# Kernel tuning notes

Hardware: AMD Instinct MI355X
Metric: run time of the kernel (lower is better)

Reference implementation:

```python
import jax, jax.numpy as jnp
import numpy as np

T, DM = 2048, 2048
H, KV, D = 16, 2, 128
E, I_MOE, I_SH = 16, 768, 768
TOP_K, N_GROUP, TOPK_GROUP = 4, 4, 2
ROPE_THETA = 1e6
EPS = 1e-5
ROUTED_SCALE = 1.0


def rmsnorm(x, w):
    v = jnp.mean(x * x, axis=-1, keepdims=True)
    return x * jax.lax.rsqrt(v + EPS) * w


def apply_rope(x, pos):
    # partial rotary: first D//2 dims rotated (neox style), rest passthrough
    rd = D // 2
    half = rd // 2
    inv = 1.0 / (ROPE_THETA ** (jnp.arange(0, rd, 2, dtype=jnp.float32) / rd))
    freqs = pos.astype(jnp.float32)[:, None] * inv  # [T, half]
    cos = jnp.cos(freqs)[:, None, :]
    sin = jnp.sin(freqs)[:, None, :]
    x1, x2 = x[..., :half], x[..., half:rd]
    rot = jnp.concatenate([x1 * cos - x2 * sin, x2 * cos + x1 * sin], axis=-1)
    return jnp.concatenate([rot, x[..., rd:]], axis=-1)


def mlp(x, wgu, wd):
    g, u = jnp.split(x @ wgu, 2, axis=-1)
    return (jax.nn.silu(g) * u) @ wd


def attention(x, pos, w_qkv, b_qkv, w_o, q_norm_w, k_norm_w):
    qkv = x @ w_qkv + b_qkv
    q, k, v = jnp.split(qkv, [H * D, H * D + KV * D], axis=-1)
    q = rmsnorm(q.reshape(T, H, D), q_norm_w)
    k = rmsnorm(k.reshape(T, KV, D), k_norm_w)
    v = v.reshape(T, KV, D)
    q = apply_rope(q, pos)
    k = apply_rope(k, pos)
    rep = H // KV
    k = jnp.repeat(k, rep, axis=1)
    v = jnp.repeat(v, rep, axis=1)
    scores = jnp.einsum('thd,shd->hts', q, k) * (D ** -0.5)
    causal = pos[:, None] >= pos[None, :]
    scores = jnp.where(causal[None], scores, jnp.finfo(scores.dtype).min)
    p = jax.nn.softmax(scores, axis=-1)
    o = jnp.einsum('hts,shd->thd', p, v).reshape(T, H * D)
    return o @ w_o


def moe(x, gate_w, gate_bias, shared_wgu, shared_wd, expert_wgu, expert_wd):
    # sigmoid grouped top-k routing with e_score_correction_bias (DeepSeek/GLM style)
    logits = x.astype(jnp.float32) @ gate_w
    scores = jax.nn.sigmoid(logits)
    sb = scores + gate_bias
    g = sb.reshape(T, N_GROUP, E // N_GROUP)
    group_scores = jnp.sum(jax.lax.top_k(g, 2)[0], axis=-1)  # [T, n_group]
    _, gi = jax.lax.top_k(group_scores, TOPK_GROUP)
    gmask = jnp.zeros((T, N_GROUP)).at[jnp.arange(T)[:, None], gi].set(1.0)
    emask = jnp.repeat(gmask, E // N_GROUP, axis=1)
    masked = jnp.where(emask > 0, sb, -jnp.inf)
    _, idx = jax.lax.top_k(masked, TOP_K)  # [T, top_k]
    w = jnp.take_along_axis(scores, idx, axis=1)
    w = w / jnp.sum(w, axis=1, keepdims=True)  # renormalize (norm_topk_prob)
    cw = jnp.zeros((T, E)).at[jnp.arange(T)[:, None], idx].add(w)  # dense combine weights
    gu = jnp.einsum('td,edi->tei', x, expert_wgu)  # [T, E, 2I]
    gt, ut = jnp.split(gu, 2, axis=-1)
    act = jax.nn.silu(gt) * ut * cw[:, :, None]
    routed = jnp.einsum('tei,eid->td', act, expert_wd)
    shared = mlp(x, shared_wgu, shared_wd)
    return routed * ROUTED_SCALE + shared


def setup_inputs() -> dict:
    key = jax.random.key(0)
    ks = jax.random.split(key, 12)
    s = 0.02
    return {
        'positions': jnp.arange(T, dtype=jnp.int32),
        'hidden_states': jax.random.normal(ks[0], (T, DM), jnp.float32),
        'residual': jax.random.normal(ks[1], (T, DM), jnp.float32),
        'ln1_w': jnp.ones((DM,), jnp.float32),
        'ln2_w': jnp.ones((DM,), jnp.float32),
        'w_qkv': jax.random.normal(ks[2], (DM, (H + 2 * KV) * D), jnp.float32) * s,
        'b_qkv': jnp.zeros(((H + 2 * KV) * D,), jnp.float32),
        'w_o': jax.random.normal(ks[3], (H * D, DM), jnp.float32) * s,
        'q_norm_w': jnp.ones((D,), jnp.float32),
        'k_norm_w': jnp.ones((D,), jnp.float32),
        'gate_w': jax.random.normal(ks[4], (DM, E), jnp.float32) * s,
        'gate_bias': jax.random.normal(ks[5], (E,), jnp.float32) * 0.1,
        'shared_wgu': jax.random.normal(ks[6], (DM, 2 * I_SH), jnp.float32) * s,
        'shared_wd': jax.random.normal(ks[7], (I_SH, DM), jnp.float32) * s,
        'expert_wgu': jax.random.normal(ks[8], (E, DM, 2 * I_MOE), jnp.float32) * s,
        'expert_wd': jax.random.normal(ks[9], (E, I_MOE, DM), jnp.float32) * s,
    }


def reference(positions, hidden_states, residual, ln1_w, ln2_w, w_qkv, b_qkv, w_o,
              q_norm_w, k_norm_w, gate_w, gate_bias, shared_wgu, shared_wd,
              expert_wgu, expert_wd):
    # fused add + RMSNorm (residual is not None path)
    residual = hidden_states + residual
    h = rmsnorm(residual, ln1_w)
    h = attention(h, positions, w_qkv, b_qkv, w_o, q_norm_w, k_norm_w)
    residual = h + residual
    h = rmsnorm(residual, ln2_w)
    h = moe(h, gate_w, gate_bias, shared_wgu, shared_wd, expert_wgu, expert_wd)
    return h, residual
```

## Files before the change

### kernel.cpp

```cpp
#include <hip/hip_runtime.h>
#include <stdint.h>
#include <math.h>

#define T_ 2048
#define DM 2048
#define NH 16
#define NKV 2
#define HD 128
#define QKVN 2560
#define NE 16
#define IM 768
#define ISH 768
#define MAXROWS 10240
#define ROWS_ALL 12288
#define NBLK 136
#define SM_SCALE 0.08838834764831845f

typedef __attribute__((ext_vector_type(8))) short short8;
typedef __attribute__((ext_vector_type(4))) float f32x4;

__device__ __forceinline__ float bf2f(unsigned short u){ return __uint_as_float(((unsigned int)u)<<16); }
__device__ __forceinline__ unsigned short f2bf(float f){
  unsigned int u = __float_as_uint(f);
  return (unsigned short)((u + 0x7FFFu + ((u>>16)&1u)) >> 16);
}
__device__ __forceinline__ void split2(float x, unsigned short& hi, unsigned short& lo){
  hi = f2bf(x);
  lo = f2bf(x - bf2f(hi));
}

__device__ __forceinline__ void gload16(const void* g, void* l){
  __builtin_amdgcn_global_load_lds((const __attribute__((address_space(1))) unsigned int*)g,
                                   (__attribute__((address_space(3))) unsigned int*)l, 16, 0, 0);
}

__device__ __forceinline__ int xcd_swz(int bid, int nwg){
  int q = nwg >> 3, r = nwg & 7, x = bid & 7, p = bid >> 3;
  return (x < r ? x*(q+1) : r*(q+1) + (x-r)*q) + p;
}

#define BAR()    asm volatile("s_barrier" ::: "memory")
#define VW(N)    asm volatile("s_waitcnt vmcnt(" #N ")" ::: "memory")
#define LW0()    do{ asm volatile("s_waitcnt lgkmcnt(0)" ::: "memory"); __builtin_amdgcn_sched_barrier(0); }while(0)

template<bool ILV>
__global__ void k_tconv(const float* __restrict__ src, unsigned short* __restrict__ dst,
                        const float* __restrict__ srcS, unsigned short* __restrict__ dstS,
                        int R, int C, size_t sS, size_t sD){
  int z = blockIdx.z;
  if (srcS && z == gridDim.z-1){ src = srcS; dst = dstS; }
  else { src += (size_t)z * sS; dst += (size_t)z * sD; }
  __shared__ float tile[64*65];
  int tid = threadIdx.x;
  int r0 = blockIdx.y*64, c0 = blockIdx.x*64;
  int lr = tid>>4, lc = (tid&15)*4;
  #pragma unroll
  for (int j=0;j<4;j++){
    int row = j*16 + lr;
    float4 v = *(const float4*)&src[(size_t)(r0+row)*C + c0 + lc];
    float* t = &tile[row*65 + lc];
    t[0]=v.x; t[1]=v.y; t[2]=v.z; t[3]=v.w;
  }
  __syncthreads();
  #pragma unroll
  for (int jj=0;jj<2;jj++){
    int slot = jj*256 + tid;
    int c = slot>>3, ro = (slot&7)*8;
    int cg = c0 + c;
    int cd = cg;
    if (ILV){ int b = cg>>3, inner = cg&7; cd = (b<96 ? b*16 : (b-96)*16+8) + inner; }
    short8 o;
    #pragma unroll
    for (int k=0;k<8;k++) o[k] = (short)f2bf(tile[(ro+k)*65 + c]);
    *(short8*)&dst[(size_t)cd*R + r0 + ro] = o;
  }
}

__global__ void k_tconv2(const float* __restrict__ src, unsigned short* __restrict__ dhi,
                         unsigned short* __restrict__ dlo, int R, int C){
  __shared__ float tile[64*65];
  int tid = threadIdx.x;
  int r0 = blockIdx.y*64, c0 = blockIdx.x*64;
  int lr = tid>>4, lc = (tid&15)*4;
  #pragma unroll
  for (int j=0;j<4;j++){
    int row = j*16 + lr;
    float4 v = *(const float4*)&src[(size_t)(r0+row)*C + c0 + lc];
    float* t = &tile[row*65 + lc];
    t[0]=v.x; t[1]=v.y; t[2]=v.z; t[3]=v.w;
  }
  __syncthreads();
  #pragma unroll
  for (int jj=0;jj<2;jj++){
    int slot = jj*256 + tid;
    int c = slot>>3, ro = (slot&7)*8;
    short8 oh, ol;
    #pragma unroll
    for (int k=0;k<8;k++){
      unsigned short h_, l_;
      split2(tile[(ro+k)*65 + c], h_, l_);
      oh[k] = (short)h_; ol[k] = (short)l_;
    }
    size_t o = (size_t)(c0+c)*R + r0 + ro;
    *(short8*)&dhi[o] = oh;
    *(short8*)&dlo[o] = ol;
  }
}

template<bool ROUTE>
__global__ void k_add_rmsnorm(const float* __restrict__ a, const float* __restrict__ b,
                              const float* __restrict__ w, float* __restrict__ resout,
                              unsigned short* __restrict__ ohi, unsigned short* __restrict__ olo,
                              unsigned short* __restrict__ obf,
                              const float* __restrict__ gw, const float* __restrict__ gbias,
                              int* __restrict__ idx4, float* __restrict__ w4){
  int t = blockIdx.x, tid = threadIdx.x;
  const float4* a4 = (const float4*)(a + (size_t)t*DM);
  const float4* b4 = (const float4*)(b + (size_t)t*DM);
  float4 va = a4[tid], vb = b4[tid];
  float4 wa = a4[tid+256], wb = b4[tid+256];
  float4 v0, v1;
  v0.x=va.x+vb.x; v0.y=va.y+vb.y; v0.z=va.z+vb.z; v0.w=va.w+vb.w;
  v1.x=wa.x+wb.x; v1.y=wa.y+wb.y; v1.z=wa.z+wb.z; v1.w=wa.w+wb.w;
  float s = v0.x*v0.x+v0.y*v0.y+v0.z*v0.z+v0.w*v0.w
          + v1.x*v1.x+v1.y*v1.y+v1.z*v1.z+v1.w*v1.w;
  #pragma unroll
  for (int o=32;o;o>>=1) s += __shfl_xor(s,o);
  __shared__ float sm[4];
  if ((tid&63)==0) sm[tid>>6]=s;
  __syncthreads();
  s = sm[0]+sm[1]+sm[2]+sm[3];
  float rs = rsqrtf(s*(1.f/(float)DM) + 1e-5f);
  ((float4*)(resout + (size_t)t*DM))[tid] = v0;
  ((float4*)(resout + (size_t)t*DM))[tid+256] = v1;
  const float4* w4p_ = (const float4*)w;
  float4 w0 = w4p_[tid], w1 = w4p_[tid+256];
  float n[8] = { v0.x*rs*w0.x, v0.y*rs*w0.y, v0.z*rs*w0.z, v0.w*rs*w0.w,
                 v1.x*rs*w1.x, v1.y*rs*w1.y, v1.z*rs*w1.z, v1.w*rs*w1.w };
  if (ohi){
    ushort4 h0,h1,l0,l1;
    split2(n[0],h0.x,l0.x); split2(n[1],h0.y,l0.y); split2(n[2],h0.z,l0.z); split2(n[3],h0.w,l0.w);
    split2(n[4],h1.x,l1.x); split2(n[5],h1.y,l1.y); split2(n[6],h1.z,l1.z); split2(n[7],h1.w,l1.w);
    ((ushort4*)(ohi + (size_t)t*DM))[tid] = h0;
    ((ushort4*)(ohi + (size_t)t*DM))[tid+256] = h1;
    ((ushort4*)(olo + (size_t)t*DM))[tid] = l0;
    ((ushort4*)(olo + (size_t)t*DM))[tid+256] = l1;
  }
  if (obf){
    ushort4 o0 = make_ushort4(f2bf(n[0]),f2bf(n[1]),f2bf(n[2]),f2bf(n[3]));
    ushort4 o1 = make_ushort4(f2bf(n[4]),f2bf(n[5]),f2bf(n[6]),f2bf(n[7]));
    ((ushort4*)(obf + (size_t)t*DM))[tid] = o0;
    ((ushort4*)(obf + (size_t)t*DM))[tid+256] = o1;
  }
  if constexpr (ROUTE){
    __shared__ float xrow[DM];
    __shared__ float red[16][17];
    #pragma unroll
    for (int jj=0;jj<4;jj++) xrow[4*tid+jj] = n[jj];
    #pragma unroll
    for (int jj=0;jj<4;jj++) xrow[1024+4*tid+jj] = n[4+jj];
    __syncthreads();
    int e = tid & 15, grp = tid >> 4;
    float part = 0.f;
    #pragma unroll 8
    for (int c = grp; c < DM; c += 16)
      part += xrow[c] * gw[(size_t)c*16 + e];
    red[grp][e] = part;
    __syncthreads();
    if (tid==0){
      float sc[16], sb[16];
      for (int ee=0;ee<16;ee++){
        float lg = 0.f;
        for (int g2=0;g2<16;g2++) lg += red[g2][ee];
        sc[ee] = 1.f/(1.f+expf(-lg));
        sb[ee] = sc[ee] + gbias[ee];
      }
      float gs[4];
      for (int g=0;g<4;g++){
        float m1=-3.4e38f, m2=-3.4e38f;
        for (int j=0;j<4;j++){
          float v = sb[g*4+j];
          if (v>m1){ m2=m1; m1=v; } else if (v>m2) m2=v;
        }
        gs[g]=m1+m2;
      }
      int g1=0; for (int g=1;g<4;g++) if (gs[g]>gs[g1]) g1=g;
      int g2=-1; for (int g=0;g<4;g++){ if (g==g1) continue; if (g2<0 || gs[g]>gs[g2]) g2=g; }
      float msk[16];
      for (int ee=0;ee<16;ee++){ int g=ee>>2; msk[ee] = (g==g1||g==g2)? sb[ee] : -3.4e38f; }
      int id[4]; float wv[4]; float wsum=0.f;
      for (int s2=0;s2<4;s2++){
        int bb=0; float bv=-3.5e38f;
        for (int ee=0;ee<16;ee++) if (msk[ee]>bv){ bv=msk[ee]; bb=ee; }
        id[s2]=bb; wv[s2]=sc[bb]; wsum+=sc[bb]; msk[bb]=-3.5e38f;
      }
      float invs = 1.f/wsum;
      for (int s2=0;s2<4;s2++){
        idx4[t*4+s2]=id[s2];
        w4[t*4+s2]=wv[s2]*invs;
      }
    }
  }
}

template<bool GATHER, bool ACT>
__global__ __launch_bounds__(256) void k_gemm2(
    const unsigned short* __restrict__ A, const unsigned short* __restrict__ Be,
    const unsigned short* __restrict__ Bsh, unsigned short* __restrict__ C,
    int K, int lda, int ldb, int ldc,
    const int* __restrict__ offs, size_t sBe, const int* __restrict__ tok){
  int nx = gridDim.x;
  int nwg = nx * gridDim.y;
  int wid_ = xcd_swz(blockIdx.x + nx*blockIdx.y, nwg);
  int tN = wid_ % nx, tM = wid_ / nx;
  int rb = tM*128;
  if (rb >= offs[17]) return;
  const unsigned short* B;
  if (rb >= offs[16]) B = Bsh;
  else {
    int e=0;
    for (; e<15; ++e) if (offs[e+1] > rb) break;
    B = Be + (size_t)e*sBe;
  }
  __shared__ __align__(16) unsigned short As[2][4096];
  __shared__ __align__(16) unsigned short Bs[2][4096];
  int tid = threadIdx.x, lane = tid & 63, wwid = tid >> 6;
  int wr = wwid >> 1, wc = wwid & 1;
  const unsigned short* Bb = B + (size_t)tN*128*ldb;

  const unsigned short* Asrc0;
  const unsigned short* Asrc1;
  int r0s = tid>>2, r1s = r0s + 64;
  {
    if (GATHER){
      Asrc0 = A + (size_t)tok[rb + r0s]*lda;
      Asrc1 = A + (size_t)tok[rb + r1s]*lda;
    } else {
      Asrc0 = A + (size_t)(rb + r0s)*lda;
      Asrc1 = A + (size_t)(rb + r1s)*lda;
    }
  }
  int kc = tid&3;
  int sw = (r0s>>1)&3;
  int kcS = (kc ^ sw)*8;

  f32x4 acc[4][4];
  #pragma unroll
  for (int m=0;m<4;m++)
    #pragma unroll
    for (int n=0;n<4;n++) acc[m][n] = (f32x4){0.f,0.f,0.f,0.f};

  auto STAGE = [&](int b, int k0){
    gload16(Asrc0 + k0 + kcS, As[b] + (size_t)tid*8);
    gload16(Asrc1 + k0 + kcS, As[b] + (size_t)(256+tid)*8);
    gload16(Bb + (size_t)r0s*ldb + k0 + kcS, Bs[b] + (size_t)tid*8);
    gload16(Bb + (size_t)r1s*ldb + k0 + kcS, Bs[b] + (size_t)(256+tid)*8);
  };

  int nt = K >> 5, L = nt - 1;
  STAGE(0, 0);
  if (L >= 1) STAGE(1, 32);
  int i15 = lane & 15, g = lane >> 4;
  for (int i=0; i<nt; ++i){
    int cur = i & 1;
    if (i < L) { VW(4); } else { VW(0); }
    BAR();
    short8 af[4], bfr[4];
    #pragma unroll
    for (int m=0;m<4;m++){
      int row = wr*64 + m*16 + i15;
      int geff = g ^ ((row>>1)&3);
      af[m] = *(const short8*)(As[cur] + row*32 + geff*8);
    }
    #pragma unroll
    for (int n=0;n<4;n++){
      int row = wc*64 + n*16 + i15;
      int geff = g ^ ((row>>1)&3);
      bfr[n] = *(const short8*)(Bs[cur] + row*32 + geff*8);
    }
    LW0();
    BAR();
    if (i + 2 <= L) STAGE(cur, (i+2)*32);
    __builtin_amdgcn_s_setprio(1);
    #pragma unroll
    for (int m=0;m<4;m++)
      #pragma unroll
      for (int n=0;n<4;n++)
        acc[m][n] = __builtin_amdgcn_mfma_f32_16x16x32_bf16(af[m], bfr[n], acc[m][n], 0,0,0);
    __builtin_amdgcn_s_setprio(0);
  }

  if (ACT){
    int rbase = rb + wr*64, cb = tN*128 + wc*64;
    #pragma unroll
    for (int m=0;m<4;m++){
      int r0 = rbase + m*16 + ((lane>>4)<<2);
      #pragma unroll
      for (int n=0;n<4;n++){
        int f = ((cb + n*16)>>1) + (lane&7);
        #pragma unroll
        for (int r=0;r<4;r++){
          float v = acc[m][n][r];
          float vp = __shfl_xor(v, 8);
          if (!(lane&8)){
            float gg = v;
            float a = gg/(1.f+__expf(-gg))*vp;
            C[(size_t)(r0+r)*ldc + f] = f2bf(a);
          }
        }
      }
    }
  } else {
    int rbase = rb + wr*64, cb = tN*128 + wc*64;
    #pragma unroll
    for (int m=0;m<4;m++){
      int r0 = rbase + m*16 + ((lane>>4)<<2);
      #pragma unroll
      for (int n=0;n<4;n++){
        int c = cb + n*16 + (lane&15);
        #pragma unroll
        for (int r=0;r<4;r++) C[(size_t)(r0+r)*ldc + c] = f2bf(acc[m][n][r]);
      }
    }
  }
}

__global__ __launch_bounds__(256) void k_gemm_hp(
    const unsigned short* __restrict__ Ah, const unsigned short* __restrict__ Al,
    const unsigned short* __restrict__ Bh, const unsigned short* __restrict__ Bl,
    float* __restrict__ Cf,
    int K, int lda, int ldb, int ldc){
  int nx = gridDim.x, nwg = nx*gridDim.y;
  int w = xcd_swz(blockIdx.x + nx*blockIdx.y, nwg);
  int tN = w % nx, tM = w / nx;

  __shared__ __align__(16) unsigned short AsH[2][4096], AsL[2][4096];
  __shared__ __align__(16) unsigned short BsH[2][4096], BsL[2][4096];
  int tid = threadIdx.x, lane = tid & 63, wid = tid >> 6;
  int wr = wid >> 1, wc = wid & 1;
  const unsigned short* Abh = Ah + (size_t)tM*128*lda;
  const unsigned short* Abl = Al + (size_t)tM*128*lda;
  const unsigned short* Bbh = Bh + (size_t)tN*128*ldb;
  const unsigned short* Bbl = Bl + (size_t)tN*128*ldb;

  f32x4 acc[4][4];
  #pragma unroll
  for (int m=0;m<4;m++)
    #pragma unroll
    for (int n=0;n<4;n++) acc[m][n] = (f32x4){0.f,0.f,0.f,0.f};

  auto STAGE = [&](int b, int k0){
    #pragma unroll
    for (int j=0;j<2;j++){
      int cb = j*256 + tid;
      int row = cb>>2, kc = cb&3;
      int kcS = (kc ^ ((row>>1)&3))*8;
      size_t go = (size_t)row*lda + k0 + kcS;
      gload16(Abh + go, AsH[b] + (size_t)cb*8);
      gload16(Abl + go, AsL[b] + (size_t)cb*8);
      size_t bo = (size_t)row*ldb + k0 + kcS;
      gload16(Bbh + bo, BsH[b] + (size_t)cb*8);
      gload16(Bbl + bo, BsL[b] + (size_t)cb*8);
    }
  };

  int nt = K >> 5, L = nt - 1;
  STAGE(0, 0);
  if (L >= 1) STAGE(1, 32);
  int i15 = lane & 15, g = lane >> 4;
  for (int i=0; i<nt; ++i){
    int cur = i & 1;
    if (i < L) { VW(8); } else { VW(0); }
    BAR();
    short8 afh[4], afl[4], bfh[4], bfl[4];
    #pragma unroll
    for (int m=0;m<4;m++){
      int row = wr*64 + m*16 + i15;
      int ro = row*32 + (g ^ ((row>>1)&3))*8;
      afh[m] = *(const short8*)(AsH[cur] + ro);
      afl[m] = *(const short8*)(AsL[cur] + ro);
    }
    #pragma unroll
    for (int n=0;n<4;n++){
      int row = wc*64 + n*16 + i15;
      int ro = row*32 + (g ^ ((row>>1)&3))*8;
      bfh[n] = *(const short8*)(BsH[cur] + ro);
      bfl[n] = *(const short8*)(BsL[cur] + ro);
    }
    LW0();
    BAR();
    if (i + 2 <= L) STAGE(cur, (i+2)*32);
    __builtin_amdgcn_s_setprio(1);
    #pragma unroll
    for (int m=0;m<4;m++)
      #pragma unroll
      for (int n=0;n<4;n++){
        acc[m][n] = __builtin_amdgcn_mfma_f32_16x16x32_bf16(afh[m], bfh[n], acc[m][n], 0,0,0);
        acc[m][n] = __builtin_amdgcn_mfma_f32_16x16x32_bf16(afh[m], bfl[n], acc[m][n], 0,0,0);
        acc[m][n] = __builtin_amdgcn_mfma_f32_16x16x32_bf16(afl[m], bfh[n], acc[m][n], 0,0,0);
      }
    __builtin_amdgcn_s_setprio(0);
  }

  int rb = tM*128 + wr*64, cb = tN*128 + wc*64;
  #pragma unroll
  for (int m=0;m<4;m++){
    int r0 = rb + m*16 + ((lane>>4)<<2);
    #pragma unroll
    for (int n=0;n<4;n++){
      int c = cb + n*16 + (lane&15);
      #pragma unroll
      for (int r=0;r<4;r++) Cf[(size_t)(r0+r)*ldc + c] = acc[m][n][r];
    }
  }
}

__global__ __launch_bounds__(256) void k_qk_pers(
    const unsigned short* __restrict__ Qh, const unsigned short* __restrict__ Ql,
    const unsigned short* __restrict__ Kh, const unsigned short* __restrict__ Kl,
    float* __restrict__ Sp){
  int tM = blockIdx.x, z = blockIdx.y;
  int kvh = z >> 3;
  size_t tri = (size_t)tM*(tM+1)/2;
  const int ldq = NH*HD, ldk = NKV*HD;
  const unsigned short* Qbh = Qh + (size_t)(tM*128)*ldq + (size_t)z*HD;
  const unsigned short* Qbl = Ql + (size_t)(tM*128)*ldq + (size_t)z*HD;
  const unsigned short* Kbh = Kh + (size_t)kvh*HD;
  const unsigned short* Kbl = Kl + (size_t)kvh*HD;

  __shared__ __align__(16) unsigned short QsH[16384], QsL[16384];
  __shared__ __align__(16) unsigned short BsH[2][4096], BsL[2][4096];

  int tid = threadIdx.x, lane = tid & 63, wid = tid >> 6;
  int wr = wid >> 1, wc = wid & 1;
  int i15 = lane & 15, g = lane >> 4;

  #pragma unroll
  for (int j=0;j<8;j++){
    int gi = j*256 + tid;
    int chunk = gi >> 9;
    int row = (gi >> 2) & 127;
    int gg = gi & 3;
    int col = chunk*32 + (gg ^ ((row>>1)&3))*8;
    gload16(Qbh + (size_t)row*ldq + col, QsH + (size_t)gi*8);
    gload16(Qbl + (size_t)row*ldq + col, QsL + (size_t)gi*8);
  }

  auto BSTAGE = [&](int b, int ci){
    int tn = ci >> 2, c = ci & 3;
    const unsigned short* sh = Kbh + (size_t)(tn*128)*ldk;
    const unsigned short* sl = Kbl + (size_t)(tn*128)*ldk;
    #pragma unroll
    for (int j=0;j<2;j++){
      int gi = j*256 + tid;
      int row = gi >> 2, gg = gi & 3;
      int col = c*32 + (gg ^ ((row>>1)&3))*8;
      gload16(sh + (size_t)row*ldk + col, BsH[b] + (size_t)gi*8);
      gload16(sl + (size_t)row*ldk + col, BsL[b] + (size_t)gi*8);
    }
  };

  f32x4 acc[4][4];
  #pragma unroll
  for (int m=0;m<4;m++)
    #pragma unroll
    for (int n=0;n<4;n++) acc[m][n] = (f32x4){0.f,0.f,0.f,0.f};

  int NC = (tM+1)*4;
  BSTAGE(0, 0);
  BSTAGE(1, 1);
  for (int ci=0; ci<NC; ++ci){
    int cur = ci & 1, c = ci & 3, tn = ci >> 2;
    if (ci < NC-1) { VW(4); } else { VW(0); }
    BAR();
    short8 afh[4], afl[4], bfh[4], bfl[4];
    #pragma unroll
    for (int m=0;m<4;m++){
      int row = wr*64 + m*16 + i15;
      int ro = c*4096 + row*32 + (g ^ ((row>>1)&3))*8;
      afh[m] = *(const short8*)(QsH + ro);
      afl[m] = *(const short8*)(QsL + ro);
    }
    #pragma unroll
    for (int n=0;n<4;n++){
      int row = wc*64 + n*16 + i15;
      int ro = row*32 + (g ^ ((row>>1)&3))*8;
      bfh[n] = *(const short8*)(BsH[cur] + ro);
      bfl[n] = *(const short8*)(BsL[cur] + ro);
    }
    LW0();
    BAR();
    if (ci + 2 < NC) BSTAGE(cur, ci+2);
    __builtin_amdgcn_s_setprio(1);
    #pragma unroll
    for (int m=0;m<4;m++)
      #pragma unroll
      for (int n=0;n<4;n++){
        acc[m][n] = __builtin_amdgcn_mfma_f32_16x16x32_bf16(afh[m], bfh[n], acc[m][n], 0,0,0);
        acc[m][n] = __builtin_amdgcn_mfma_f32_16x16x32_bf16(afh[m], bfl[n], acc[m][n], 0,0,0);
        acc[m][n] = __builtin_amdgcn_mfma_f32_16x16x32_bf16(afl[m], bfh[n], acc[m][n], 0,0,0);
      }
    __builtin_amdgcn_s_setprio(0);
    if (c == 3){
      float* Cb = Sp + ((size_t)z*NBLK + tri + tn)*16384;
      #pragma unroll
      for (int m=0;m<4;m++){
        int r0 = wr*64 + m*16 + (g<<2);
        #pragma unroll
        for (int n=0;n<4;n++){
          int ccol = wc*64 + n*16 + i15;
          #pragma unroll
          for (int r=0;r<4;r++) Cb[(size_t)(r0+r)*128 + ccol] = acc[m][n][r];
        }
      }
      #pragma unroll
      for (int m=0;m<4;m++)
        #pragma unroll
        for (int n=0;n<4;n++) acc[m][n] = (f32x4){0.f,0.f,0.f,0.f};
    }
  }
}

__global__ void k_softmax_ml(float* __restrict__ Sp, float* __restrict__ mlb){
  int t = blockIdx.x, h = blockIdx.y, tid = threadIdx.x;
  int tM = t>>7, tr = t&127;
  size_t base = ((size_t)h*NBLK + (size_t)tM*(tM+1)/2)*16384 + (size_t)tr*128;
  int nv = t+1, kc = (tM+1)<<7;
  __shared__ float sm[4];
  float rv[8];
  #pragma unroll
  for (int j=0;j<8;j++){
    int s = tid + j*256;
    rv[j] = (s<nv) ? Sp[base + (size_t)(s>>7)*16384 + (s&127)]*SM_SCALE : -1e30f;
  }
  float m = rv[0];
  #pragma unroll
  for (int j=1;j<8;j++) m = fmaxf(m, rv[j]);
  #pragma unroll
  for (int o=32;o;o>>=1) m = fmaxf(m, __shfl_xor(m,o));
  if ((tid&63)==0) sm[tid>>6]=m;
  __syncthreads();
  m = fmaxf(fmaxf(sm[0],sm[1]),fmaxf(sm[2],sm[3]));
  __syncthreads();
  float sum = 0.f;
  #pragma unroll
  for (int j=0;j<8;j++) sum += __expf(rv[j]-m);
  #pragma unroll
  for (int o=32;o;o>>=1) sum += __shfl_xor(sum,o);
  if ((tid&63)==0) sm[tid>>6]=sum;
  __syncthreads();
  sum = sm[0]+sm[1]+sm[2]+sm[3];
  if (tid==0) mlb[(size_t)h*T_ + t] = m + logf(sum);
  for (int s = nv + tid; s < kc; s += 256)
    Sp[base + (size_t)(s>>7)*16384 + (s&127)] = -1e30f;
}

__global__ __launch_bounds__(256) void k_pv_hp(
    const float* __restrict__ Sp, const float* __restrict__ mlb,
    const unsigned short* __restrict__ Vh, const unsigned short* __restrict__ Vl,
    float* __restrict__ part){
  int c = blockIdx.x, tM = blockIdx.y, z = blockIdx.z;
  int kbeg = c*512;
  int kend = min((tM+1)*128, (c+1)*512);
  if (kbeg >= kend) return;
  size_t tri = (size_t)tM*(tM+1)/2;
  const float* Ab = Sp + ((size_t)z*NBLK + tri)*16384;
  const unsigned short* Bbh = Vh + (size_t)(z>>3)*HD*T_;
  const unsigned short* Bbl = Vl + (size_t)(z>>3)*HD*T_;

  __shared__ __align__(16) float Asf[2][4096];
  __shared__ __align__(16) unsigned short BsH[2][4096], BsL[2][4096];
  int tid = threadIdx.x, lane = tid & 63, wid = tid >> 6;
  int wr = wid >> 1, wc = wid & 1;
  int i15 = lane & 15, g2 = (lane>>4)*2;

  float mrow[4];
  #pragma unroll
  for (int m=0;m<4;m++)
    mrow[m] = mlb[(size_t)z*T_ + tM*128 + wr*64 + m*16 + i15];

  int r0s = tid>>2, r1s = r0s + 64;
  int kcB = ((tid&3) ^ ((r0s>>1)&3))*8;
  int rowA = tid>>3, gA = tid&7;

  f32x4 acc[4][4];
  #pragma unroll
  for (int m=0;m<4;m++)
    #pragma unroll
    for (int n=0;n<4;n++) acc[m][n] = (f32x4){0.f,0.f,0.f,0.f};

  auto STAGE = [&](int b, int k0){
    #pragma unroll
    for (int j=0;j<4;j++){
      int r = j*32 + rowA;
      int gS = gA ^ (r & 7);
      size_t ga = (size_t)(k0>>7)*16384 + (size_t)r*128 + (k0&127) + gS*4;
      gload16(Ab + ga, Asf[b] + ((size_t)j*256 + tid)*4);
    }
    size_t bo0 = (size_t)r0s*T_ + k0 + kcB;
    size_t bo1 = (size_t)r1s*T_ + k0 + kcB;
    gload16(Bbh + bo0, BsH[b] + (size_t)tid*8);
    gload16(Bbh + bo1, BsH[b] + (size_t)(256+tid)*8);
    gload16(Bbl + bo0, BsL[b] + (size_t)tid*8);
    gload16(Bbl + bo1, BsL[b] + (size_t)(256+tid)*8);
  };

  int nt = (kend - kbeg) >> 5, L = nt - 1;
  STAGE(0, kbeg);
  if (L >= 1) STAGE(1, kbeg + 32);
  for (int i=0; i<nt; ++i){
    int cur = i & 1;
    if (i < L) { VW(8); } else { VW(0); }
    BAR();
    short8 afh[4], afl[4], bfh[4], bfl[4];
    #pragma unroll
    for (int m=0;m<4;m++){
      int r = wr*64 + m*16 + i15;
      int s0 = r*8 + ((g2  ) ^ (r&7));
      int s1 = r*8 + ((g2+1) ^ (r&7));
      f32x4 a0 = *(const f32x4*)(Asf[cur] + s0*4);
      f32x4 a1 = *(const f32x4*)(Asf[cur] + s1*4);
      float pv[8] = {a0[0],a0[1],a0[2],a0[3],a1[0],a1[1],a1[2],a1[3]};
      short8 h8, l8;
      #pragma unroll
      for (int j=0;j<8;j++){
        float p = __expf(pv[j]*SM_SCALE - mrow[m]);
        unsigned short hh, ll; split2(p, hh, ll);
        h8[j] = (short)hh; l8[j] = (short)ll;
      }
      afh[m] = h8; afl[m] = l8;
    }
    #pragma unroll
    for (int n=0;n<4;n++){
      int row = wc*64 + n*16 + i15;
      int ro = row*32 + ((lane>>4) ^ ((row>>1)&3))*8;
      bfh[n] = *(const short8*)(BsH[cur] + ro);
      bfl[n] = *(const short8*)(BsL[cur] + ro);
    }
    LW0();
    BAR();
    if (i + 2 <= L) STAGE(cur, kbeg + (i+2)*32);
    __builtin_amdgcn_s_setprio(1);
    #pragma unroll
    for (int m=0;m<4;m++)
      #pragma unroll
      for (int n=0;n<4;n++){
        acc[m][n] = __builtin_amdgcn_mfma_f32_16x16x32_bf16(afh[m], bfh[n], acc[m][n], 0,0,0);
        acc[m][n] = __builtin_amdgcn_mfma_f32_16x16x32_bf16(afh[m], bfl[n], acc[m][n], 0,0,0);
        acc[m][n] = __builtin_amdgcn_mfma_f32_16x16x32_bf16(afl[m], bfh[n], acc[m][n], 0,0,0);
      }
    __builtin_amdgcn_s_setprio(0);
  }

  float* Cb = part + (size_t)c*T_*DM + (size_t)tM*128*DM + (size_t)z*HD;
  #pragma unroll
  for (int m=0;m<4;m++){
    int r0 = wr*64 + m*16 + ((lane>>4)<<2);
    #pragma unroll
    for (int n=0;n<4;n++){
      int ccol = wc*64 + n*16 + (lane&15);
      #pragma unroll
      for (int r=0;r<4;r++) Cb[(size_t)(r0+r)*DM + ccol] = acc[m][n][r];
    }
  }
}

__global__ void k_pv_reduce(const float* __restrict__ part,
                            unsigned short* __restrict__ aoh, unsigned short* __restrict__ aol){
  int t = blockIdx.x, tid = threadIdx.x;
  int nc = ((t>>7) + 4) >> 2;
  #pragma unroll
  for (int half=0; half<2; ++half){
    int idx = tid + half*256;
    float4 s = ((const float4*)(part + (size_t)t*DM))[idx];
    for (int c=1; c<nc; ++c){
      float4 v = ((const float4*)(part + (size_t)c*T_*DM + (size_t)t*DM))[idx];
      s.x+=v.x; s.y+=v.y; s.z+=v.z; s.w+=v.w;
    }
    ushort4 h_, l_;
    split2(s.x,h_.x,l_.x); split2(s.y,h_.y,l_.y); split2(s.z,h_.z,l_.z); split2(s.w,h_.w,l_.w);
    ((ushort4*)(aoh + (size_t)t*DM))[idx] = h_;
    ((ushort4*)(aol + (size_t)t*DM))[idx] = l_;
  }
}

__global__ void k_qkv_post_hp(const float* __restrict__ qkv, const float* __restrict__ bias,
                              const float* __restrict__ qnw, const float* __restrict__ knw,
                              const int* __restrict__ pos_,
                              unsigned short* __restrict__ qhi, unsigned short* __restrict__ qlo,
                              unsigned short* __restrict__ khi, unsigned short* __restrict__ klo,
                              unsigned short* __restrict__ vThi, unsigned short* __restrict__ vTlo){
  int t = blockIdx.x;
  int half = threadIdx.x >> 7;
  int d = threadIdx.x & 127;
  int wseg = (threadIdx.x >> 6) & 1;
  float posf = (float)pos_[t];
  __shared__ float buf[2][128];
  __shared__ float ssum[2][2];
  __shared__ float inv_sh[32];
  if (threadIdx.x < 32)
    inv_sh[threadIdx.x] = (float)pow(1000000.0, -(double)threadIdx.x/32.0);
  __syncthreads();
  for (int it=0; it<10; ++it){
    int seg = it*2 + half;
    float x = qkv[(size_t)t*QKVN + seg*128 + d] + bias[seg*128 + d];
    float p = x*x;
    #pragma unroll
    for (int o=32;o;o>>=1) p += __shfl_xor(p,o);
    if ((threadIdx.x&63)==0) ssum[half][wseg] = p;
    __syncthreads();
    float rs = rsqrtf((ssum[half][0]+ssum[half][1])*(1.f/128.f) + 1e-5f);
    float w = (seg<16) ? qnw[d] : ((seg<18) ? knw[d] : 1.f);
    float nv = x*rs*w;
    buf[half][d] = nv;
    __syncthreads();
    float outv = (seg<18) ? nv : x;
    if (seg < 18 && d < 64){
      int i = d & 31;
      float ang = posf * inv_sh[i];
      float sn, cs; sincosf(ang, &sn, &cs);
      if (d < 32) outv = nv*cs - buf[half][d+32]*sn;
      else        outv = nv*cs + buf[half][d-32]*sn;
    }
    unsigned short h_, l_; split2(outv, h_, l_);
    if (seg < 16){ size_t o = ((size_t)t*NH + seg)*HD + d; qhi[o]=h_; qlo[o]=l_; }
    else if (seg < 18){ size_t o = ((size_t)t*NKV + (seg-16))*HD + d; khi[o]=h_; klo[o]=l_; }
    else { size_t o = ((size_t)(seg-18)*HD + d)*T_ + t; vThi[o]=h_; vTlo[o]=l_; }
    __syncthreads();
  }
}

__global__ void k_offsets(const int* __restrict__ idx4, int* __restrict__ offs,
                          int* __restrict__ fill){
  __shared__ int hist[16];
  if (threadIdx.x < 16) hist[threadIdx.x] = 0;
  __syncthreads();
  for (int i = threadIdx.x; i < T_*4; i += 256)
    atomicAdd(&hist[idx4[i]], 1);
  __syncthreads();
  fill[threadIdx.x] = 0;
  if (threadIdx.x == 0){
    int o = 0;
    for (int e=0;e<16;e++){ offs[e]=o; o += ((hist[e]+127)>>7)<<7; }
    offs[16]=o;
    offs[17]=o + T_;
  }
}

__global__ void k_place(const int* __restrict__ idx4, const int* __restrict__ offs,
                        int* __restrict__ fill, int* __restrict__ rrow, int* __restrict__ tok){
  int t = blockIdx.x*256 + threadIdx.x;
  if (t>=T_) return;
  for (int s=0;s<4;s++){
    int e = idx4[t*4+s];
    int p = atomicAdd(&fill[e*16],1);
    int r = offs[e]+p;
    rrow[t*4+s]=r;
    tok[r]=t;
  }
  tok[offs[16]+t] = t;
}

__global__ void k_combine(const unsigned short* __restrict__ eout,
                          const int* __restrict__ rrow, const float* __restrict__ w4,
                          const int* __restrict__ offs, float* __restrict__ outh){
  int t = blockIdx.x;
  int rs = offs[16] + t;
  int r0=rrow[t*4+0], r1=rrow[t*4+1], r2=rrow[t*4+2], r3=rrow[t*4+3];
  float w0=w4[t*4+0], w1=w4[t*4+1], w2=w4[t*4+2], w3=w4[t*4+3];
  for (int d=threadIdx.x; d<DM; d+=256){
    float v = bf2f(eout[(size_t)rs*DM+d])
            + w0*bf2f(eout[(size_t)r0*DM+d]) + w1*bf2f(eout[(size_t)r1*DM+d])
            + w2*bf2f(eout[(size_t)r2*DM+d]) + w3*bf2f(eout[(size_t)r3*DM+d]);
    outh[(size_t)t*DM+d] = v;
  }
}

extern "C" void kernel_launch(void* const* d_in, const int* in_sizes, int n_in,
                              void* d_out, int out_size, void* d_ws, size_t ws_size,
                              hipStream_t stream){
  const int*   positions = (const int*)d_in[0];
  const float* hidden    = (const float*)d_in[1];
  const float* residual  = (const float*)d_in[2];
  const float* ln1       = (const float*)d_in[3];
  const float* ln2       = (const float*)d_in[4];
  const float* w_qkv     = (const float*)d_in[5];
  const float* b_qkv     = (const float*)d_in[6];
  const float* w_o       = (const float*)d_in[7];
  const float* qnw       = (const float*)d_in[8];
  const float* knw       = (const float*)d_in[9];
  const float* gate_w    = (const float*)d_in[10];
  const float* gate_b    = (const float*)d_in[11];
  const float* sh_wgu    = (const float*)d_in[12];
  const float* sh_wd     = (const float*)d_in[13];
  const float* e_wgu     = (const float*)d_in[14];
  const float* e_wd      = (const float*)d_in[15];
  float* out_h   = (float*)d_out;
  float* out_res = (float*)d_out + (size_t)T_*DM;

  char* ws = (char*)d_ws;
  size_t off = 0;
  auto alloc = [&](size_t b){ size_t r = off; off += (b + 255) & ~(size_t)255; return r; };

  size_t o_h2b  = alloc((size_t)T_*DM*2);
  size_t o_idx  = alloc((size_t)T_*4*4);
  size_t o_w4   = alloc((size_t)T_*4*4);
  size_t o_offs = alloc(72);
  size_t o_fill = alloc(1024);
  size_t o_rrow = alloc((size_t)T_*4*4);
  size_t o_tok  = alloc((size_t)ROWS_ALL*4);

  size_t U0 = off;
  size_t a = U0;
  auto allocA = [&](size_t b){ size_t r = a; a += (b + 255) & ~(size_t)255; return r; };
  size_t o_h1h  = allocA((size_t)T_*DM*2);
  size_t o_h1l  = allocA((size_t)T_*DM*2);
  size_t o_wqh  = allocA((size_t)QKVN*DM*2);
  size_t o_wql  = allocA((size_t)QKVN*DM*2);
  size_t o_qkvf = allocA((size_t)T_*QKVN*4);
  size_t o_qh   = allocA((size_t)T_*NH*HD*2);
  size_t o_ql   = allocA((size_t)T_*NH*HD*2);
  size_t o_kh   = allocA((size_t)T_*NKV*HD*2);
  size_t o_kl   = allocA((size_t)T_*NKV*HD*2);
  size_t o_vth  = allocA((size_t)NKV*HD*T_*2);
  size_t o_vtl  = allocA((size_t)NKV*HD*T_*2);
  size_t o_woh  = allocA((size_t)DM*DM*2);
  size_t o_wol  = allocA((size_t)DM*DM*2);
  size_t o_aoh  = allocA((size_t)T_*DM*2);
  size_t o_aol  = allocA((size_t)T_*DM*2);
  size_t o_attnP= allocA((size_t)T_*DM*4);
  size_t o_mlb  = allocA((size_t)NH*T_*4);
  size_t o_Sp   = allocA((size_t)NH*NBLK*16384*4);
  size_t o_pvp  = allocA((size_t)4*T_*DM*4);
  size_t b_ = U0;
  auto allocB = [&](size_t b){ size_t r = b_; b_ += (b + 255) & ~(size_t)255; return r; };
  size_t o_ewgu = allocB((size_t)NE*2*IM*DM*2);
  size_t o_ewd  = allocB((size_t)NE*DM*IM*2);
  size_t o_shgu = allocB((size_t)2*ISH*DM*2);
  size_t o_shwd = allocB((size_t)DM*ISH*2);
  size_t o_actx = allocB((size_t)ROWS_ALL*IM*2);
  size_t o_eout = allocB((size_t)ROWS_ALL*DM*2);

  unsigned short* h2b   = (unsigned short*)(ws+o_h2b);
  int*   idx4  = (int*)(ws+o_idx);
  float* w4p   = (float*)(ws+o_w4);
  int*   offs  = (int*)(ws+o_offs);
  int*   fill  = (int*)(ws+o_fill);
  int*   rrow  = (int*)(ws+o_rrow);
  int*   tok   = (int*)(ws+o_tok);
  unsigned short* h1h = (unsigned short*)(ws+o_h1h);
  unsigned short* h1l = (unsigned short*)(ws+o_h1l);
  unsigned short* wqh = (unsigned short*)(ws+o_wqh);
  unsigned short* wql = (unsigned short*)(ws+o_wql);
  float*          qkvf= (float*)(ws+o_qkvf);
  unsigned short* qh  = (unsigned short*)(ws+o_qh);
  unsigned short* ql  = (unsigned short*)(ws+o_ql);
  unsigned short* kh  = (unsigned short*)(ws+o_kh);
  unsigned short* kl  = (unsigned short*)(ws+o_kl);
  unsigned short* vth = (unsigned short*)(ws+o_vth);
  unsigned short* vtl = (unsigned short*)(ws+o_vtl);
  unsigned short* woh = (unsigned short*)(ws+o_woh);
  unsigned short* wol = (unsigned short*)(ws+o_wol);
  unsigned short* aoh = (unsigned short*)(ws+o_aoh);
  unsigned short* aol = (unsigned short*)(ws+o_aol);
  float*          attnP=(float*)(ws+o_attnP);
  float*          mlb = (float*)(ws+o_mlb);
  float*          Sp  = (float*)(ws+o_Sp);
  float*          pvpart = (float*)(ws+o_pvp);
  unsigned short* ewguT=(unsigned short*)(ws+o_ewgu);
  unsigned short* ewdT = (unsigned short*)(ws+o_ewd);
  unsigned short* shguT=(unsigned short*)(ws+o_shgu);
  unsigned short* shwdT=(unsigned short*)(ws+o_shwd);
  unsigned short* actx= (unsigned short*)(ws+o_actx);
  unsigned short* eout= (unsigned short*)(ws+o_eout);

  hipMemsetAsync(tok, 0, (size_t)ROWS_ALL*4, stream);

  k_tconv2<<<dim3(QKVN/64, DM/64, 1),256,0,stream>>>(w_qkv, wqh, wql, DM, QKVN);
  k_tconv2<<<dim3(DM/64, DM/64, 1),256,0,stream>>>(w_o, woh, wol, DM, DM);

  k_add_rmsnorm<false><<<T_,256,0,stream>>>(hidden, residual, ln1, out_res, h1h, h1l, nullptr,
                                            nullptr, nullptr, nullptr, nullptr);

  k_gemm_hp<<<dim3(QKVN/128,T_/128,1),256,0,stream>>>(
      h1h, h1l, wqh, wql, qkvf, DM, DM, DM, QKVN);
  k_qkv_post_hp<<<T_,256,0,stream>>>(qkvf, b_qkv, qnw, knw, positions, qh, ql, kh, kl, vth, vtl);

  k_qk_pers<<<dim3(T_/128,NH),256,0,stream>>>(qh, ql, kh, kl, Sp);
  k_softmax_ml<<<dim3(T_,NH),256,0,stream>>>(Sp, mlb);
  k_pv_hp<<<dim3(4,T_/128,NH),256,0,stream>>>(Sp, mlb, vth, vtl, pvpart);
  k_pv_reduce<<<T_,256,0,stream>>>(pvpart, aoh, aol);
  k_gemm_hp<<<dim3(DM/128,T_/128,1),256,0,stream>>>(
      aoh, aol, woh, wol, attnP, DM, DM, DM, DM);

  k_add_rmsnorm<true><<<T_,256,0,stream>>>(attnP, out_res, ln2, out_res, nullptr, nullptr, h2b,
                                           gate_w, gate_b, idx4, w4p);

  k_offsets<<<1,256,0,stream>>>(idx4, offs, fill);
  k_place<<<T_/256,256,0,stream>>>(idx4, offs, fill, rrow, tok);

  k_tconv<true ><<<dim3(2*IM/64, DM/64, NE+1),256,0,stream>>>(
      e_wgu, ewguT, sh_wgu, shguT, DM, 2*IM, (size_t)DM*2*IM, (size_t)2*IM*DM);
  k_tconv<false><<<dim3(DM/64, IM/64, NE+1),256,0,stream>>>(
      e_wd,  ewdT,  sh_wd,  shwdT, IM, DM,   (size_t)IM*DM,   (size_t)DM*IM);

  k_gemm2<true, true ><<<dim3(2*IM/128, ROWS_ALL/128, 1),256,0,stream>>>(
      h2b, ewguT, shguT, actx, DM, DM, DM, IM, offs, (size_t)2*IM*DM, tok);
  k_gemm2<false, false><<<dim3(DM/128, ROWS_ALL/128, 1),256,0,stream>>>(
      actx, ewdT, shwdT, eout, IM, IM, IM, DM, offs, (size_t)DM*IM, nullptr);

  k_combine<<<T_,256,0,stream>>>(eout, rrow, w4p, offs, out_h);
}
```

Measured before the change: 751.2 us.

## Fuse softmax row statistics into QK kernel epilogue and mask causally in PV

The QK score kernel now computes per-row partial max and sum-of-exp for each 128x64 half-tile in its epilogue and writes them to small buffers. A light combine kernel merges these partials into the log-sum-exp, replacing the separate softmax pass that re-read the whole score matrix and wrote -inf into the masked diagonal entries. Causal masking moves into the PV kernel's diagonal tiles instead. The memset of the token buffer is also folded into the offsets kernel, removing one launch. The QK epilogue gains extra shuffles and exp work, and the new partial buffers add some memory traffic.

```diff
diff --git a/kernel.cpp b/kernel.cpp
--- a/kernel.cpp
+++ b/kernel.cpp
@@ -418,7 +418,7 @@
 __global__ __launch_bounds__(256) void k_qk_pers(
     const unsigned short* __restrict__ Qh, const unsigned short* __restrict__ Ql,
     const unsigned short* __restrict__ Kh, const unsigned short* __restrict__ Kl,
-    float* __restrict__ Sp){
+    float* __restrict__ Sp, float* __restrict__ mpart, float* __restrict__ lpart){
   int tM = blockIdx.x, z = blockIdx.y;
   int kvh = z >> 3;
   size_t tri = (size_t)tM*(tM+1)/2;
@@ -513,6 +513,40 @@
           for (int r=0;r<4;r++) Cb[(size_t)(r0+r)*128 + ccol] = acc[m][n][r];
         }
       }
+      int diag = (tn == tM);
+      #pragma unroll
+      for (int m=0;m<4;m++){
+        #pragma unroll
+        for (int r=0;r<4;r++){
+          int rl = wr*64 + m*16 + (g<<2) + r;
+          float vmax = -3.0e38f;
+          #pragma unroll
+          for (int n=0;n<4;n++){
+            int cl = wc*64 + n*16 + i15;
+            float v = acc[m][n][r]*SM_SCALE;
+            if (diag && cl > rl) v = -3.0e38f;
+            vmax = fmaxf(vmax, v);
+          }
+          #pragma unroll
+          for (int o=1;o<16;o<<=1) vmax = fmaxf(vmax, __shfl_xor(vmax, o));
+          float s = 0.f;
+          #pragma unroll
+          for (int n=0;n<4;n++){
+            int cl = wc*64 + n*16 + i15;
+            float v = acc[m][n][r]*SM_SCALE;
+            float e = (diag && cl > rl) ? 0.f : __expf(v - vmax);
+            s += e;
+          }
+          #pragma unroll
+          for (int o=1;o<16;o<<=1) s += __shfl_xor(s, o);
+          if ((lane&15)==0){
+            int rg = tM*128 + rl;
+            size_t o = (((size_t)z*T_ + rg)*16 + tn)*2 + wc;
+            mpart[o] = vmax;
+            lpart[o] = s;
+          }
+        }
+      }
       #pragma unroll
       for (int m=0;m<4;m++)
         #pragma unroll
@@ -521,38 +555,19 @@
   }
 }
 
-__global__ void k_softmax_ml(float* __restrict__ Sp, float* __restrict__ mlb){
-  int t = blockIdx.x, h = blockIdx.y, tid = threadIdx.x;
-  int tM = t>>7, tr = t&127;
-  size_t base = ((size_t)h*NBLK + (size_t)tM*(tM+1)/2)*16384 + (size_t)tr*128;
-  int nv = t+1, kc = (tM+1)<<7;
-  __shared__ float sm[4];
-  float rv[8];
-  #pragma unroll
-  for (int j=0;j<8;j++){
-    int s = tid + j*256;
-    rv[j] = (s<nv) ? Sp[base + (size_t)(s>>7)*16384 + (s&127)]*SM_SCALE : -1e30f;
-  }
-  float m = rv[0];
-  #pragma unroll
-  for (int j=1;j<8;j++) m = fmaxf(m, rv[j]);
-  #pragma unroll
-  for (int o=32;o;o>>=1) m = fmaxf(m, __shfl_xor(m,o));
-  if ((tid&63)==0) sm[tid>>6]=m;
-  __syncthreads();
-  m = fmaxf(fmaxf(sm[0],sm[1]),fmaxf(sm[2],sm[3]));
-  __syncthreads();
-  float sum = 0.f;
-  #pragma unroll
-  for (int j=0;j<8;j++) sum += __expf(rv[j]-m);
-  #pragma unroll
-  for (int o=32;o;o>>=1) sum += __shfl_xor(sum,o);
-  if ((tid&63)==0) sm[tid>>6]=sum;
-  __syncthreads();
-  sum = sm[0]+sm[1]+sm[2]+sm[3];
-  if (tid==0) mlb[(size_t)h*T_ + t] = m + logf(sum);
-  for (int s = nv + tid; s < kc; s += 256)
-    Sp[base + (size_t)(s>>7)*16384 + (s&127)] = -1e30f;
+__global__ void k_mlcombine(const float* __restrict__ mpart, const float* __restrict__ lpart,
+                            float* __restrict__ mlb){
+  int idx = blockIdx.x*256 + threadIdx.x;
+  if (idx >= NH*T_) return;
+  int t = idx & (T_-1);
+  int nb = ((t>>7)+1)*2;
+  const float* mp = mpart + (size_t)idx*32;
+  const float* lp = lpart + (size_t)idx*32;
+  float m = -3.0e38f;
+  for (int i=0;i<nb;i++) m = fmaxf(m, mp[i]);
+  float l = 0.f;
+  for (int i=0;i<nb;i++) l += lp[i]*__expf(mp[i]-m);
+  mlb[idx] = m + logf(l);
 }
 
 __global__ __launch_bounds__(256) void k_pv_hp(
@@ -563,6 +578,7 @@
   int kbeg = c*512;
   int kend = min((tM+1)*128, (c+1)*512);
   if (kbeg >= kend) return;
+  int tMk = tM*128;
   size_t tri = (size_t)tM*(tM+1)/2;
   const float* Ab = Sp + ((size_t)z*NBLK + tri)*16384;
   const unsigned short* Bbh = Vh + (size_t)(z>>3)*HD*T_;
@@ -577,7 +593,7 @@
   float mrow[4];
   #pragma unroll
   for (int m=0;m<4;m++)
-    mrow[m] = mlb[(size_t)z*T_ + tM*128 + wr*64 + m*16 + i15];
+    mrow[m] = mlb[(size_t)z*T_ + tMk + wr*64 + m*16 + i15];
 
   int r0s = tid>>2, r1s = r0s + 64;
   int kcB = ((tid&3) ^ ((r0s>>1)&3))*8;
@@ -610,8 +626,10 @@
   if (L >= 1) STAGE(1, kbeg + 32);
   for (int i=0; i<nt; ++i){
     int cur = i & 1;
+    int k0 = kbeg + i*32;
     if (i < L) { VW(8); } else { VW(0); }
     BAR();
+    int diag = (k0 >= tMk);
     short8 afh[4], afl[4], bfh[4], bfl[4];
     #pragma unroll
     for (int m=0;m<4;m++){
@@ -621,6 +639,14 @@
       f32x4 a0 = *(const f32x4*)(Asf[cur] + s0*4);
       f32x4 a1 = *(const f32x4*)(Asf[cur] + s1*4);
       float pv[8] = {a0[0],a0[1],a0[2],a0[3],a1[0],a1[1],a1[2],a1[3]};
+      if (diag){
+        int kb = k0 & 127;
+        #pragma unroll
+        for (int j=0;j<8;j++){
+          int kl = kb + ((j<4) ? g2*4 + j : (g2+1)*4 + (j-4));
+          if (kl > r) pv[j] = -3.0e38f;
+        }
+      }
       short8 h8, l8;
       #pragma unroll
       for (int j=0;j<8;j++){
@@ -652,7 +678,7 @@
     __builtin_amdgcn_s_setprio(0);
   }
 
-  float* Cb = part + (size_t)c*T_*DM + (size_t)tM*128*DM + (size_t)z*HD;
+  float* Cb = part + (size_t)c*T_*DM + (size_t)tMk*DM + (size_t)z*HD;
   #pragma unroll
   for (int m=0;m<4;m++){
     int r0 = wr*64 + m*16 + ((lane>>4)<<2);
@@ -731,10 +757,11 @@
 }
 
 __global__ void k_offsets(const int* __restrict__ idx4, int* __restrict__ offs,
-                          int* __restrict__ fill){
+                          int* __restrict__ fill, int* __restrict__ tok){
   __shared__ int hist[16];
   if (threadIdx.x < 16) hist[threadIdx.x] = 0;
   __syncthreads();
+  for (int i = threadIdx.x; i < ROWS_ALL; i += 256) tok[i] = 0;
   for (int i = threadIdx.x; i < T_*4; i += 256)
     atomicAdd(&hist[idx4[i]], 1);
   __syncthreads();
@@ -830,6 +857,8 @@
   size_t o_aol  = allocA((size_t)T_*DM*2);
   size_t o_attnP= allocA((size_t)T_*DM*4);
   size_t o_mlb  = allocA((size_t)NH*T_*4);
+  size_t o_mpart= allocA((size_t)NH*T_*32*4);
+  size_t o_lpart= allocA((size_t)NH*T_*32*4);
   size_t o_Sp   = allocA((size_t)NH*NBLK*16384*4);
   size_t o_pvp  = allocA((size_t)4*T_*DM*4);
   size_t b_ = U0;
@@ -865,6 +894,8 @@
   unsigned short* aol = (unsigned short*)(ws+o_aol);
   float*          attnP=(float*)(ws+o_attnP);
   float*          mlb = (float*)(ws+o_mlb);
+  float*          mpart=(float*)(ws+o_mpart);
+  float*          lpart=(float*)(ws+o_lpart);
   float*          Sp  = (float*)(ws+o_Sp);
   float*          pvpart = (float*)(ws+o_pvp);
   unsigned short* ewguT=(unsigned short*)(ws+o_ewgu);
@@ -874,8 +905,6 @@
   unsigned short* actx= (unsigned short*)(ws+o_actx);
   unsigned short* eout= (unsigned short*)(ws+o_eout);
 
-  hipMemsetAsync(tok, 0, (size_t)ROWS_ALL*4, stream);
-
   k_tconv2<<<dim3(QKVN/64, DM/64, 1),256,0,stream>>>(w_qkv, wqh, wql, DM, QKVN);
   k_tconv2<<<dim3(DM/64, DM/64, 1),256,0,stream>>>(w_o, woh, wol, DM, DM);
 
@@ -886,8 +915,8 @@
       h1h, h1l, wqh, wql, qkvf, DM, DM, DM, QKVN);
   k_qkv_post_hp<<<T_,256,0,stream>>>(qkvf, b_qkv, qnw, knw, positions, qh, ql, kh, kl, vth, vtl);
 
-  k_qk_pers<<<dim3(T_/128,NH),256,0,stream>>>(qh, ql, kh, kl, Sp);
-  k_softmax_ml<<<dim3(T_,NH),256,0,stream>>>(Sp, mlb);
+  k_qk_pers<<<dim3(T_/128,NH),256,0,stream>>>(qh, ql, kh, kl, Sp, mpart, lpart);
+  k_mlcombine<<<(NH*T_+255)/256,256,0,stream>>>(mpart, lpart, mlb);
   k_pv_hp<<<dim3(4,T_/128,NH),256,0,stream>>>(Sp, mlb, vth, vtl, pvpart);
   k_pv_reduce<<<T_,256,0,stream>>>(pvpart, aoh, aol);
   k_gemm_hp<<<dim3(DM/128,T_/128,1),256,0,stream>>>(
@@ -896,7 +925,7 @@
   k_add_rmsnorm<true><<<T_,256,0,stream>>>(attnP, out_res, ln2, out_res, nullptr, nullptr, h2b,
                                            gate_w, gate_b, idx4, w4p);
 
-  k_offsets<<<1,256,0,stream>>>(idx4, offs, fill);
+  k_offsets<<<1,256,0,stream>>>(idx4, offs, fill, tok);
   k_place<<<T_/256,256,0,stream>>>(idx4, offs, fill, rrow, tok);
 
   k_tconv<true ><<<dim3(2*IM/64, DM/64, NE+1),256,0,stream>>>(
```

Result: slower. 832.3 us (+10.8%).
